# Performance work log

Hardware: AMD Instinct MI355X
Metric: run time of the kernel (lower is better)

Reference implementation:

```python
import jax, jax.numpy as jnp
import numpy as np

N_NODES = 260000          # 10,000 graphs * 26 nodes/graph (split size hardcoded in Net)
N_EDGES = 8320000         # avg degree 32
GRAPH_NODES = 26
IN_DIM, H1, H2 = 4, 26, 11
POOL_OUT = 4              # MaxPool1d(3, stride=3, padding=1) on 11 channels -> 4


def setup_inputs() -> dict:
    key = jax.random.key(0)
    ks = jax.random.split(key, 8)
    x = jax.random.normal(ks[0], (N_NODES, IN_DIM), dtype=jnp.float32)
    edge_index = jax.random.randint(ks[1], (2, N_EDGES), 0, N_NODES, dtype=jnp.int32)
    W1 = jax.random.normal(ks[2], (H1, IN_DIM), dtype=jnp.float32) * 0.3
    b1 = jax.random.normal(ks[3], (H1,), dtype=jnp.float32) * 0.1
    W2 = jax.random.normal(ks[4], (H2, H1), dtype=jnp.float32) * 0.2
    b2 = jax.random.normal(ks[5], (H2,), dtype=jnp.float32) * 0.1
    Wl = jax.random.normal(ks[6], (2, POOL_OUT), dtype=jnp.float32) * 0.3
    bl = jax.random.normal(ks[7], (2,), dtype=jnp.float32) * 0.1
    return {"x": x, "edge_index": edge_index, "W1": W1, "b1": b1,
            "W2": W2, "b2": b2, "Wl": Wl, "bl": bl}


def reference(x, edge_index, W1, b1, W2, b2, Wl, bl):
    N = x.shape[0]
    # add_self_loops
    loops = jnp.arange(N, dtype=edge_index.dtype)
    row = jnp.concatenate([edge_index[0], loops])
    col = jnp.concatenate([edge_index[1], loops])

    def gcn(h, W, b):
        h = h @ W.T + b                       # Linear
        # message: deg = ones -> norm = 1, so message is just x_j = h[row]
        # aggr='add': scatter-add into target nodes (col)
        return jax.ops.segment_sum(h[row], col, num_segments=N)

    h = jnp.tanh(gcn(x, W1, b1))              # [N, 26]
    h = jnp.tanh(gcn(h, W2, b2))              # [N, 11]

    # MaxPool1d(kernel=3, stride=3, padding=1) over the 11 channels -> 4.
    # Left pad by 1 with -inf; the right pad element is never inside a window.
    neg = jnp.full((N, 1), -jnp.inf, dtype=h.dtype)
    hp = jnp.concatenate([neg, h], axis=1)    # [N, 12]
    pooled = hp.reshape(N, POOL_OUT, 3).max(axis=2)  # [N, 4]

    # graph pooling: sum every consecutive block of 26 nodes
    g = pooled.reshape(-1, GRAPH_NODES, POOL_OUT).sum(axis=1)  # [G, 4]

    out = g @ Wl.T + bl                        # [G, 2]
    return jax.nn.softmax(out, axis=-1)        # F.softmax default dim=1 for 2D
```

## Files before the change

kernel.cpp:

```cpp
#include <hip/hip_runtime.h>
#include <hip/hip_fp16.h>

#define N_NODES 260000
#define N_EDGES 8320000
#define H1 26
#define H2 11
#define GRAPH_NODES 26
#define N_GRAPHS 10000

#define NB 128
#define NBUCK 2032
#define NPB 256
#define PBT 1024
#define EPB 32500
#define ZS 16
#define FSTRIDE 13

__device__ __forceinline__ float2 up2(unsigned u) {
    __half2 h = *reinterpret_cast<const __half2*>(&u);
    return __half22float2(h);
}
__device__ __forceinline__ unsigned pk2(float a, float b) {
    __half2 h = __floats2half2_rn(a, b);
    return *reinterpret_cast<const unsigned*>(&h);
}

__global__ __launch_bounds__(256) void zero_kernel(unsigned* __restrict__ ghist,
                                                   float* __restrict__ gpool) {
    int i = blockIdx.x * 256 + threadIdx.x;
    if (i < NBUCK) ghist[i] = 0u;
    if (i < N_GRAPHS * 4) gpool[i] = 0.f;
}

__global__ __launch_bounds__(PBT) void count_kernel(const int* __restrict__ col,
                                                    unsigned* __restrict__ ghist) {
    __shared__ unsigned lh[NBUCK];
    for (int b = threadIdx.x; b < NBUCK; b += PBT) lh[b] = 0u;
    __syncthreads();
    int e0 = blockIdx.x * EPB, e1 = e0 + EPB;
    for (int e = e0 + threadIdx.x; e < e1; e += PBT)
        atomicAdd(&lh[((unsigned)col[e]) >> 7], 1u);
    __syncthreads();
    for (int b = threadIdx.x; b < NBUCK; b += PBT)
        if (lh[b]) atomicAdd(&ghist[b], lh[b]);
}

__global__ __launch_bounds__(1024) void scan_kernel(const unsigned* __restrict__ ghist,
                                                    unsigned* __restrict__ bstart,
                                                    unsigned* __restrict__ bfill) {
    __shared__ unsigned v[2048];
    int t = threadIdx.x;
    int t1 = t + 1024;
    v[t]  = (t  < NBUCK) ? ghist[t]  : 0u;
    v[t1] = (t1 < NBUCK) ? ghist[t1] : 0u;
    __syncthreads();
    for (int off = 1; off < 2048; off <<= 1) {
        unsigned a0 = (t  >= off) ? v[t  - off] : 0u;
        unsigned a1 = (t1 >= off) ? v[t1 - off] : 0u;
        __syncthreads();
        v[t]  += a0;
        v[t1] += a1;
        __syncthreads();
    }
    if (t < NBUCK) {
        unsigned st = (t == 0) ? 0u : v[t - 1];
        bstart[t] = st; bfill[t] = st;
    }
    if (t1 < NBUCK) {
        unsigned st = v[t1 - 1];
        bstart[t1] = st; bfill[t1] = st;
        if (t1 == NBUCK - 1) bstart[NBUCK] = v[t1];
    }
}

__global__ __launch_bounds__(PBT) void place_kernel(const int* __restrict__ row,
                                                    const int* __restrict__ col,
                                                    unsigned* __restrict__ bfill,
                                                    unsigned* __restrict__ part) {
    __shared__ unsigned lh[NBUCK];
    __shared__ unsigned lbase[NBUCK];
    for (int b = threadIdx.x; b < NBUCK; b += PBT) lh[b] = 0u;
    __syncthreads();
    int e0 = blockIdx.x * EPB, e1 = e0 + EPB;
    for (int e = e0 + threadIdx.x; e < e1; e += PBT)
        atomicAdd(&lh[((unsigned)col[e]) >> 7], 1u);
    __syncthreads();
    for (int b = threadIdx.x; b < NBUCK; b += PBT) {
        unsigned c = lh[b];
        lbase[b] = c ? atomicAdd(&bfill[b], c) : 0u;
    }
    __syncthreads();
    for (int b = threadIdx.x; b < NBUCK; b += PBT) lh[b] = 0u;
    __syncthreads();
    for (int e = e0 + threadIdx.x; e < e1; e += PBT) {
        unsigned c = (unsigned)col[e];
        unsigned b = c >> 7;
        unsigned p = lbase[b] + atomicAdd(&lh[b], 1u);
        part[p] = (((unsigned)row[e]) << 7) | (c & 127u);
    }
}

__device__ __forceinline__ void acc_node(float* acc, unsigned cl, float4 xv) {
    float* a = acc + cl * 5;
    atomicAdd(&a[0], xv.x); atomicAdd(&a[1], xv.y);
    atomicAdd(&a[2], xv.z); atomicAdd(&a[3], xv.w);
    atomicAdd(&a[4], 1.f);
}

__global__ __launch_bounds__(256) void layer1_kernel(const unsigned* __restrict__ part,
                                                     const unsigned* __restrict__ bstart,
                                                     const float* __restrict__ x,
                                                     const float* __restrict__ W1,
                                                     const float* __restrict__ b1,
                                                     const float* __restrict__ W2,
                                                     const float* __restrict__ b2,
                                                     ushort* __restrict__ zmsg) {
    __shared__ float acc[NB * 5];
    __shared__ float sW1[H1 * 4], sb1[H1], sW2[H2 * H1];
    for (int t = threadIdx.x; t < H1 * 4; t += 256) sW1[t] = W1[t];
    for (int t = threadIdx.x; t < H1; t += 256) sb1[t] = b1[t];
    for (int t = threadIdx.x; t < H2 * H1; t += 256) sW2[t] = W2[t];
    for (int t = threadIdx.x; t < NB * 5; t += 256) acc[t] = 0.f;
    __syncthreads();
    unsigned s = bstart[blockIdx.x], e = bstart[blockIdx.x + 1];
    unsigned i = s + threadIdx.x;
    for (; i + 256 < e; i += 512) {
        unsigned u1 = part[i], u2 = part[i + 256];
        unsigned r1 = u1 >> 7, cl1 = u1 & 127u;
        unsigned r2 = u2 >> 7, cl2 = u2 & 127u;
        float4 x1 = ((const float4*)x)[r1];
        float4 x2 = ((const float4*)x)[r2];
        acc_node(acc, cl1, x1);
        acc_node(acc, cl2, x2);
    }
    if (i < e) {
        unsigned u = part[i];
        acc_node(acc, u & 127u, ((const float4*)x)[u >> 7]);
    }
    __syncthreads();
    int base = blockIdx.x * NB;
    for (int n = threadIdx.x; n < NB; n += 256) {
        int node = base + n;
        if (node >= N_NODES) continue;
        float4 xv = ((const float4*)x)[node];
        float sx = acc[n*5+0] + xv.x, sy = acc[n*5+1] + xv.y;
        float sz = acc[n*5+2] + xv.z, sw = acc[n*5+3] + xv.w;
        float deg = acc[n*5+4] + 1.f;
        float h[H1];
        #pragma unroll
        for (int j = 0; j < H1; ++j)
            h[j] = tanhf(sb1[j] * deg + sx * sW1[j*4+0] + sy * sW1[j*4+1]
                                      + sz * sW1[j*4+2] + sw * sW1[j*4+3]);
        float z[H2];
        #pragma unroll
        for (int jj = 0; jj < H2; ++jj) {
            float v = 0.f;
            #pragma unroll
            for (int k = 0; k < H1; ++k) v += h[k] * sW2[jj*H1 + k];
            z[jj] = v;
        }
        uint4 lo, hi;
        lo.x = pk2(z[0], z[1]);  lo.y = pk2(z[2], z[3]);
        lo.z = pk2(z[4], z[5]);  lo.w = pk2(z[6], z[7]);
        hi.x = pk2(z[8], z[9]);  hi.y = pk2(z[10], deg);
        hi.z = 0u; hi.w = 0u;
        uint4* zp = (uint4*)(zmsg + (size_t)node * ZS);
        zp[0] = lo;
        zp[1] = hi;
    }
}

__device__ __forceinline__ void acc_edge(float* facc, unsigned cl, uint4 A, uint2 B) {
    float* f = facc + cl * FSTRIDE;
    float2 v;
    v = up2(A.x); atomicAdd(&f[0], v.x); atomicAdd(&f[1], v.y);
    v = up2(A.y); atomicAdd(&f[2], v.x); atomicAdd(&f[3], v.y);
    v = up2(A.z); atomicAdd(&f[4], v.x); atomicAdd(&f[5], v.y);
    v = up2(A.w); atomicAdd(&f[6], v.x); atomicAdd(&f[7], v.y);
    v = up2(B.x); atomicAdd(&f[8], v.x); atomicAdd(&f[9], v.y);
    v = up2(B.y); atomicAdd(&f[10], v.x);
}

__global__ __launch_bounds__(256) void layer2_kernel(const unsigned* __restrict__ part,
                                                     const unsigned* __restrict__ bstart,
                                                     const ushort* __restrict__ zmsg,
                                                     const float* __restrict__ b2,
                                                     float* __restrict__ gpool) {
    __shared__ float facc[NB * FSTRIDE];
    __shared__ float sb2[H2];
    __shared__ float gacc[7][4];
    if (threadIdx.x < H2) sb2[threadIdx.x] = b2[threadIdx.x];
    if (threadIdx.x < 28) ((float*)gacc)[threadIdx.x] = 0.f;
    __syncthreads();
    int base = blockIdx.x * NB;
    for (int n = threadIdx.x; n < NB; n += 256) {
        const ushort* zp = zmsg + (size_t)(base + n) * ZS;
        uint4 A = *(const uint4*)zp;
        uint2 B = *(const uint2*)(zp + 8);
        float2 vd = up2(B.y);
        float deg = vd.y;
        float* f = facc + n * FSTRIDE;
        float2 v;
        v = up2(A.x); f[0] = v.x + deg*sb2[0]; f[1] = v.y + deg*sb2[1];
        v = up2(A.y); f[2] = v.x + deg*sb2[2]; f[3] = v.y + deg*sb2[3];
        v = up2(A.z); f[4] = v.x + deg*sb2[4]; f[5] = v.y + deg*sb2[5];
        v = up2(A.w); f[6] = v.x + deg*sb2[6]; f[7] = v.y + deg*sb2[7];
        v = up2(B.x); f[8] = v.x + deg*sb2[8]; f[9] = v.y + deg*sb2[9];
        f[10] = vd.x + deg*sb2[10];
    }
    __syncthreads();
    unsigned s = bstart[blockIdx.x], e = bstart[blockIdx.x + 1];
    unsigned i = s + threadIdx.x;
    for (; i + 256 < e; i += 512) {
        unsigned u1 = part[i], u2 = part[i + 256];
        unsigned r1 = u1 >> 7, cl1 = u1 & 127u;
        unsigned r2 = u2 >> 7, cl2 = u2 & 127u;
        const ushort* p1 = zmsg + (size_t)r1 * ZS;
        const ushort* p2 = zmsg + (size_t)r2 * ZS;
        uint4 A1 = *(const uint4*)p1; uint2 B1 = *(const uint2*)(p1 + 8);
        uint4 A2 = *(const uint4*)p2; uint2 B2 = *(const uint2*)(p2 + 8);
        acc_edge(facc, cl1, A1, B1);
        acc_edge(facc, cl2, A2, B2);
    }
    if (i < e) {
        unsigned u = part[i];
        unsigned r = u >> 7, cl = u & 127u;
        const ushort* p = zmsg + (size_t)r * ZS;
        uint4 A = *(const uint4*)p; uint2 B = *(const uint2*)(p + 8);
        acc_edge(facc, cl, A, B);
    }
    __syncthreads();
    int gfirst = base / GRAPH_NODES;
    int lastnode = min(base + NB - 1, N_NODES - 1);
    int glast = lastnode / GRAPH_NODES;
    for (int n = threadIdx.x; n < NB; n += 256) {
        int node = base + n;
        if (node >= N_NODES) continue;
        const float* h = facc + n * FSTRIDE;
        float p0 = tanhf(fmaxf(h[0], h[1]));
        float p1 = tanhf(fmaxf(fmaxf(h[2], h[3]), h[4]));
        float p2 = tanhf(fmaxf(fmaxf(h[5], h[6]), h[7]));
        float p3 = tanhf(fmaxf(fmaxf(h[8], h[9]), h[10]));
        int lg = node / GRAPH_NODES - gfirst;
        atomicAdd(&gacc[lg][0], p0);
        atomicAdd(&gacc[lg][1], p1);
        atomicAdd(&gacc[lg][2], p2);
        atomicAdd(&gacc[lg][3], p3);
    }
    __syncthreads();
    int ng = glast - gfirst + 1;
    for (int t = threadIdx.x; t < ng * 4; t += 256) {
        int lg = t >> 2, c = t & 3;
        float v = gacc[lg][c];
        if (v != 0.f) atomicAdd(&gpool[(size_t)(gfirst + lg) * 4 + c], v);
    }
}

__global__ __launch_bounds__(256) void final_kernel(const float* __restrict__ gpool,
                                                    const float* __restrict__ Wl,
                                                    const float* __restrict__ bl,
                                                    float* __restrict__ out) {
    int g = blockIdx.x * 256 + threadIdx.x;
    if (g >= N_GRAPHS) return;
    float4 p = ((const float4*)gpool)[g];
    float o0 = bl[0] + p.x * Wl[0] + p.y * Wl[1] + p.z * Wl[2] + p.w * Wl[3];
    float o1 = bl[1] + p.x * Wl[4] + p.y * Wl[5] + p.z * Wl[6] + p.w * Wl[7];
    float m = fmaxf(o0, o1);
    float e0 = expf(o0 - m), e1 = expf(o1 - m);
    float s = e0 + e1;
    out[g * 2 + 0] = e0 / s;
    out[g * 2 + 1] = e1 / s;
}

extern "C" void kernel_launch(void* const* d_in, const int* in_sizes, int n_in,
                              void* d_out, int out_size, void* d_ws, size_t ws_size,
                              hipStream_t stream) {
    const float* x  = (const float*)d_in[0];
    const int* ei   = (const int*)d_in[1];
    const float* W1 = (const float*)d_in[2];
    const float* b1 = (const float*)d_in[3];
    const float* W2 = (const float*)d_in[4];
    const float* b2 = (const float*)d_in[5];
    const float* Wl = (const float*)d_in[6];
    const float* bl = (const float*)d_in[7];
    float* out = (float*)d_out;

    const int* row = ei;
    const int* col = ei + N_EDGES;

    ushort*   zmsg   = (ushort*)d_ws;
    unsigned* part   = (unsigned*)((char*)d_ws + (size_t)NBUCK * NB * ZS * 2);
    unsigned* bstart = part + N_EDGES;
    unsigned* bfill  = bstart + NBUCK + 1;
    unsigned* ghist  = bfill + NBUCK;
    float*    gpool  = (float*)(ghist + NBUCK);

    zero_kernel<<<(N_GRAPHS*4 + 255)/256, 256, 0, stream>>>(ghist, gpool);
    count_kernel<<<NPB, PBT, 0, stream>>>(col, ghist);
    scan_kernel<<<1, 1024, 0, stream>>>(ghist, bstart, bfill);
    place_kernel<<<NPB, PBT, 0, stream>>>(row, col, bfill, part);
    layer1_kernel<<<NBUCK, 256, 0, stream>>>(part, bstart, x, W1, b1, W2, b2, zmsg);
    layer2_kernel<<<NBUCK, 256, 0, stream>>>(part, bstart, zmsg, b2, gpool);
    final_kernel<<<(N_GRAPHS + 255)/256, 256, 0, stream>>>(gpool, Wl, bl, out);
}
```

Before: 1.003 ms.

## Add nontemporal loads/stores and source-range-phased gather in layer2

Streaming accesses to col, row and part and the zmsg stores now use nontemporal hints, so they do not evict reusable data from cache. Layer2 preloads up to 24 edges per thread into registers and processes them in three passes by source-node range, so gathers from zmsg concentrate on about a third of the table at a time and stay cache-resident. The cost is extra register pressure, redundant range checks on each pass, and a fallback loop for buckets with more than 6144 edges.

```diff
diff --git a/kernel.cpp b/kernel.cpp
--- a/kernel.cpp
+++ b/kernel.cpp
@@ -15,6 +15,15 @@
 #define EPB 32500
 #define ZS 16
 #define FSTRIDE 13
+#define EREG 24
+
+#define TB1 86668u
+#define TB2 173336u
+
+#define NTL(p) __builtin_nontemporal_load(p)
+
+typedef unsigned int u32x4 __attribute__((ext_vector_type(4)));
+typedef unsigned int u32x2 __attribute__((ext_vector_type(2)));
 
 __device__ __forceinline__ float2 up2(unsigned u) {
     __half2 h = *reinterpret_cast<const __half2*>(&u);
@@ -39,7 +48,7 @@
     __syncthreads();
     int e0 = blockIdx.x * EPB, e1 = e0 + EPB;
     for (int e = e0 + threadIdx.x; e < e1; e += PBT)
-        atomicAdd(&lh[((unsigned)col[e]) >> 7], 1u);
+        atomicAdd(&lh[((unsigned)NTL(&col[e])) >> 7], 1u);
     __syncthreads();
     for (int b = threadIdx.x; b < NBUCK; b += PBT)
         if (lh[b]) atomicAdd(&ghist[b], lh[b]);
@@ -83,7 +92,7 @@
     __syncthreads();
     int e0 = blockIdx.x * EPB, e1 = e0 + EPB;
     for (int e = e0 + threadIdx.x; e < e1; e += PBT)
-        atomicAdd(&lh[((unsigned)col[e]) >> 7], 1u);
+        atomicAdd(&lh[((unsigned)NTL(&col[e])) >> 7], 1u);
     __syncthreads();
     for (int b = threadIdx.x; b < NBUCK; b += PBT) {
         unsigned c = lh[b];
@@ -93,10 +102,11 @@
     for (int b = threadIdx.x; b < NBUCK; b += PBT) lh[b] = 0u;
     __syncthreads();
     for (int e = e0 + threadIdx.x; e < e1; e += PBT) {
-        unsigned c = (unsigned)col[e];
+        unsigned c = (unsigned)NTL(&col[e]);
+        unsigned r = (unsigned)NTL(&row[e]);
         unsigned b = c >> 7;
         unsigned p = lbase[b] + atomicAdd(&lh[b], 1u);
-        part[p] = (((unsigned)row[e]) << 7) | (c & 127u);
+        __builtin_nontemporal_store((r << 7) | (c & 127u), &part[p]);
     }
 }
 
@@ -125,7 +135,7 @@
     unsigned s = bstart[blockIdx.x], e = bstart[blockIdx.x + 1];
     unsigned i = s + threadIdx.x;
     for (; i + 256 < e; i += 512) {
-        unsigned u1 = part[i], u2 = part[i + 256];
+        unsigned u1 = NTL(&part[i]), u2 = NTL(&part[i + 256]);
         unsigned r1 = u1 >> 7, cl1 = u1 & 127u;
         unsigned r2 = u2 >> 7, cl2 = u2 & 127u;
         float4 x1 = ((const float4*)x)[r1];
@@ -134,7 +144,7 @@
         acc_node(acc, cl2, x2);
     }
     if (i < e) {
-        unsigned u = part[i];
+        unsigned u = NTL(&part[i]);
         acc_node(acc, u & 127u, ((const float4*)x)[u >> 7]);
     }
     __syncthreads();
@@ -159,18 +169,18 @@
             for (int k = 0; k < H1; ++k) v += h[k] * sW2[jj*H1 + k];
             z[jj] = v;
         }
-        uint4 lo, hi;
+        u32x4 lo;
+        u32x2 hi;
         lo.x = pk2(z[0], z[1]);  lo.y = pk2(z[2], z[3]);
         lo.z = pk2(z[4], z[5]);  lo.w = pk2(z[6], z[7]);
         hi.x = pk2(z[8], z[9]);  hi.y = pk2(z[10], deg);
-        hi.z = 0u; hi.w = 0u;
-        uint4* zp = (uint4*)(zmsg + (size_t)node * ZS);
-        zp[0] = lo;
-        zp[1] = hi;
-    }
-}
-
-__device__ __forceinline__ void acc_edge(float* facc, unsigned cl, uint4 A, uint2 B) {
+        ushort* zp = zmsg + (size_t)node * ZS;
+        __builtin_nontemporal_store(lo, (u32x4*)zp);
+        __builtin_nontemporal_store(hi, (u32x2*)(zp + 8));
+    }
+}
+
+__device__ __forceinline__ void acc_edge(float* facc, unsigned cl, u32x4 A, u32x2 B) {
     float* f = facc + cl * FSTRIDE;
     float2 v;
     v = up2(A.x); atomicAdd(&f[0], v.x); atomicAdd(&f[1], v.y);
@@ -195,8 +205,8 @@
     int base = blockIdx.x * NB;
     for (int n = threadIdx.x; n < NB; n += 256) {
         const ushort* zp = zmsg + (size_t)(base + n) * ZS;
-        uint4 A = *(const uint4*)zp;
-        uint2 B = *(const uint2*)(zp + 8);
+        u32x4 A = *(const u32x4*)zp;
+        u32x2 B = *(const u32x2*)(zp + 8);
         float2 vd = up2(B.y);
         float deg = vd.y;
         float* f = facc + n * FSTRIDE;
@@ -210,23 +220,35 @@
     }
     __syncthreads();
     unsigned s = bstart[blockIdx.x], e = bstart[blockIdx.x + 1];
-    unsigned i = s + threadIdx.x;
-    for (; i + 256 < e; i += 512) {
-        unsigned u1 = part[i], u2 = part[i + 256];
-        unsigned r1 = u1 >> 7, cl1 = u1 & 127u;
-        unsigned r2 = u2 >> 7, cl2 = u2 & 127u;
-        const ushort* p1 = zmsg + (size_t)r1 * ZS;
-        const ushort* p2 = zmsg + (size_t)r2 * ZS;
-        uint4 A1 = *(const uint4*)p1; uint2 B1 = *(const uint2*)(p1 + 8);
-        uint4 A2 = *(const uint4*)p2; uint2 B2 = *(const uint2*)(p2 + 8);
-        acc_edge(facc, cl1, A1, B1);
-        acc_edge(facc, cl2, A2, B2);
-    }
-    if (i < e) {
+    unsigned ed[EREG];
+    #pragma unroll
+    for (int k = 0; k < EREG; ++k) {
+        unsigned idx = s + threadIdx.x + (unsigned)k * 256u;
+        ed[k] = (idx < e) ? NTL(&part[idx]) : 0xFFFFFFFFu;
+    }
+    const unsigned lob[4] = {0u, TB1, TB2, (unsigned)N_NODES};
+    #pragma unroll
+    for (int ps = 0; ps < 3; ++ps) {
+        unsigned lo = lob[ps], hi = lob[ps + 1];
+        #pragma unroll
+        for (int k = 0; k < EREG; ++k) {
+            unsigned u = ed[k];
+            unsigned r = u >> 7;
+            if (r >= lo && r < hi) {
+                unsigned cl = u & 127u;
+                const ushort* p = zmsg + (size_t)r * ZS;
+                u32x4 A = *(const u32x4*)p;
+                u32x2 B = *(const u32x2*)(p + 8);
+                acc_edge(facc, cl, A, B);
+            }
+        }
+    }
+    for (unsigned i = s + threadIdx.x + EREG * 256u; i < e; i += 256u) {
         unsigned u = part[i];
         unsigned r = u >> 7, cl = u & 127u;
         const ushort* p = zmsg + (size_t)r * ZS;
-        uint4 A = *(const uint4*)p; uint2 B = *(const uint2*)(p + 8);
+        u32x4 A = *(const u32x4*)p;
+        u32x2 B = *(const u32x2*)(p + 8);
         acc_edge(facc, cl, A, B);
     }
     __syncthreads();
```

New measurement: 1.153 ms. +14.9%, slower.
